# Performance work log

Hardware: AMD Instinct MI355X
Metric: run time of the kernel (lower is better)

Reference implementation:

```python
import jax, jax.numpy as jnp
import numpy as np

N = 50000      # nodes
DEG = 12       # in-degree per node
E = N * DEG    # 600000 edges
IN_FEATS = 256
H_FEATS = 128
NUM_LAYERS = 2
BN_EPS = 1e-5
PD_EPS = 1e-6  # torch pairwise_distance eps


def _batch_norm(x):
    # BatchNorm1d(affine=False) in training mode: per-feature batch stats, biased var
    m = x.mean(axis=0)
    v = ((x - m) ** 2).mean(axis=0)
    return (x - m) / jnp.sqrt(v + BN_EPS)


def setup_inputs() -> dict:
    key = jax.random.key(0)
    ks = jax.random.split(key, 6)
    x = jax.random.normal(ks[0], (N, IN_FEATS), dtype=jnp.float32)
    # xavier-uniform-like scales
    s_init = float(np.sqrt(6.0 / (IN_FEATS + H_FEATS)))
    s_h = float(np.sqrt(6.0 / (2 * H_FEATS)))
    W_init = jax.random.uniform(ks[1], (IN_FEATS, H_FEATS), jnp.float32, -s_init, s_init)
    W0 = jax.random.uniform(ks[2], (H_FEATS, H_FEATS), jnp.float32, -s_h, s_h)
    W1 = jax.random.uniform(ks[3], (H_FEATS, H_FEATS), jnp.float32, -s_h, s_h)
    b0 = jnp.zeros((H_FEATS,), jnp.float32)
    b1 = jnp.zeros((H_FEATS,), jnp.float32)
    src = jax.random.randint(ks[4], (E,), 0, N, dtype=jnp.int32)
    dst = jnp.repeat(jnp.arange(N, dtype=jnp.int32), DEG)  # every node has in-degree DEG
    return {"x": x, "W_init": W_init, "W0": W0, "b0": b0, "W1": W1, "b1": b1,
            "src": src, "dst": dst}


def _embed_nodes(x, W_init, Ws, bs, src, dst):
    # h = act(norm(x @ init_weight)); then GraphConv(norm='none') layers
    h = jax.nn.relu(_batch_norm(x @ W_init))
    for W, b in zip(Ws, bs):
        msg = h[src] @ W                       # [E, H]
        agg = jax.ops.segment_sum(msg, dst, num_segments=N)  # sum aggregation
        h = jax.nn.relu(_batch_norm(agg + b))
    return h


def _nonparametric_embedding(x, src, dst, deg):
    # GIN(apply_func=None, eps=-1, aggregator='mean') == mean of in-neighbors
    h = jax.nn.relu(_batch_norm(x))
    for _ in range(NUM_LAYERS):
        agg = jax.ops.segment_sum(h[src], dst, num_segments=N) / deg[:, None]
        h = jax.nn.relu(_batch_norm(agg))
    return h


def _mean_edge_dist(h, src, dst, deg):
    # apply_edges: pairwise_distance(src, dst); pull: scatter-mean onto dst
    d = jnp.linalg.norm(h[src] - h[dst] + PD_EPS, axis=1)  # [E]
    return jax.ops.segment_sum(d, dst, num_segments=N) / deg  # [N]


def reference(x, W_init, W0, b0, W1, b1, src, dst):
    deg = jnp.maximum(
        jax.ops.segment_sum(jnp.ones((E,), jnp.float32), dst, num_segments=N), 1.0)
    h_final = _embed_nodes(x, W_init, (W0, W1), (b0, b1), src, dst)
    # nonparametric target distances (detached in original)
    h_nonpar = _nonparametric_embedding(jax.lax.stop_gradient(x), src, dst, deg)
    d_nonpar = jax.lax.stop_gradient(_mean_edge_dist(h_nonpar, src, dst, deg))
    d_par = _mean_edge_dist(h_final, src, dst, deg)
    loss = jnp.mean((jnp.log(d_par) - jnp.log(d_nonpar)) ** 2)
    return (h_final, loss)
```

## Files before the change

### kernel.cpp

```cpp
#include <hip/hip_runtime.h>
#include <hip/hip_fp16.h>
#include <math.h>

#define DEG 12
#define BN_EPS 1e-5f
#define PD_EPS 1e-6f

using uint = unsigned int;

typedef _Float16 fp16x8 __attribute__((ext_vector_type(8)));
typedef float f32x2 __attribute__((ext_vector_type(2)));
typedef float f32x4 __attribute__((ext_vector_type(4)));

__device__ inline float2 h2f2(uint u) {
  __half2 h; __builtin_memcpy(&h, &u, 4);
  return __half22float2(h);
}
__device__ inline uint f2h2(float a, float b) {
  __half2 h = __floats2half2_rn(a, b);
  uint u; __builtin_memcpy(&u, &h, 4);
  return u;
}
__device__ inline f32x2 q2f_lo(uint u) { return __builtin_amdgcn_cvt_pk_f32_fp8(u, false); }
__device__ inline f32x2 q2f_hi(uint u) { return __builtin_amdgcn_cvt_pk_f32_fp8(u, true); }
__device__ inline uint f4_to_q(float a, float b, float c, float d) {
  uint w = 0;
  w = __builtin_amdgcn_cvt_pk_fp8_f32(a, b, w, false);
  w = __builtin_amdgcn_cvt_pk_fp8_f32(c, d, w, true);
  return w;
}

#define STATS_NB 256

template<int F>
__global__ __launch_bounds__(512) void stats_q_part(const uint* __restrict__ in,
                                                    float* __restrict__ parts, int M) {
  const int G = F / 8;
  __shared__ float redA[512 * 8];
  __shared__ float redB[512 * 8];
  int tid = threadIdx.x;
  int total = M * G;
  float s[8] = {0,0,0,0,0,0,0,0}, q[8] = {0,0,0,0,0,0,0,0};
  for (int i = blockIdx.x * 512 + tid; i < total; i += gridDim.x * 512) {
    uint2 raw = ((const uint2*)in)[i];
    f32x2 a = q2f_lo(raw.x), b = q2f_hi(raw.x), c = q2f_lo(raw.y), d = q2f_hi(raw.y);
    float v[8] = {a.x, a.y, b.x, b.y, c.x, c.y, d.x, d.y};
#pragma unroll
    for (int j = 0; j < 8; ++j) { s[j] += v[j]; q[j] += v[j] * v[j]; }
  }
#pragma unroll
  for (int j = 0; j < 8; ++j) { redA[tid * 8 + j] = s[j]; redB[tid * 8 + j] = q[j]; }
  __syncthreads();
  if (tid < F) {
    int c = tid >> 3, j = tid & 7;
    float as = 0.f, aq = 0.f;
#pragma unroll 4
    for (int r = 0; r < 512 / G; ++r) {
      as += redA[(r * G + c) * 8 + j];
      aq += redB[(r * G + c) * 8 + j];
    }
    parts[blockIdx.x * 2 * F + tid]     = as;
    parts[blockIdx.x * 2 * F + F + tid] = aq;
  }
}

template<int F>
__global__ __launch_bounds__(512) void stats_f_part(const float* __restrict__ in,
                                                    float* __restrict__ parts, int M) {
  const int G = F / 4;
  __shared__ float redA[512 * 4];
  __shared__ float redB[512 * 4];
  int tid = threadIdx.x;
  int total = M * G;
  float s[4] = {0,0,0,0}, q[4] = {0,0,0,0};
  for (int i = blockIdx.x * 512 + tid; i < total; i += gridDim.x * 512) {
    float4 v = ((const float4*)in)[i];
    float w[4] = {v.x, v.y, v.z, v.w};
#pragma unroll
    for (int j = 0; j < 4; ++j) { s[j] += w[j]; q[j] += w[j] * w[j]; }
  }
#pragma unroll
  for (int j = 0; j < 4; ++j) { redA[tid * 4 + j] = s[j]; redB[tid * 4 + j] = q[j]; }
  __syncthreads();
  if (tid < F) {
    int c = tid >> 2, j = tid & 3;
    float as = 0.f, aq = 0.f;
#pragma unroll 4
    for (int r = 0; r < 512 / G; ++r) {
      as += redA[(r * G + c) * 4 + j];
      aq += redB[(r * G + c) * 4 + j];
    }
    parts[blockIdx.x * 2 * F + tid]     = as;
    parts[blockIdx.x * 2 * F + F + tid] = aq;
  }
}

template<int F>
__global__ __launch_bounds__(1024) void stats_final(const float* __restrict__ parts,
                                                    int nb, int M, float* __restrict__ stats) {
  const int OUT = 2 * F;
  const int T   = 1024 / OUT;
  __shared__ float red[1024];
  int tid = threadIdx.x;
  int o = tid & (OUT - 1);
  int c = tid / OUT;
  float s = 0.f;
#pragma unroll 16
  for (int b = c; b < nb; b += T) s += parts[(size_t)b * OUT + o];
  red[tid] = s;
  __syncthreads();
  if (tid < OUT) {
    float acc = red[tid];
#pragma unroll
    for (int cc = 1; cc < T; ++cc) acc += red[cc * OUT + tid];
    red[tid] = acc;
  }
  __syncthreads();
  if (tid < F) {
    float mean = red[tid] / (float)M;
    float var  = red[F + tid] / (float)M - mean * mean;
    stats[tid]     = mean;
    stats[F + tid] = 1.0f / sqrtf(var + BN_EPS);
  }
}

__global__ void transpose_all(const float* __restrict__ Wi, const float* __restrict__ W0,
                              const float* __restrict__ W1, __half* __restrict__ WiT,
                              __half* __restrict__ W0T, __half* __restrict__ W1T) {
  int idx = blockIdx.x * 256 + threadIdx.x;
  if (idx < 32768) {
    int n = idx / 256, k = idx - n * 256;
    WiT[idx] = __float2half(Wi[(size_t)k * 128 + n]);
  } else if (idx < 49152) {
    int i = idx - 32768; int n = i / 128, k = i - n * 128;
    W0T[i] = __float2half(W0[(size_t)k * 128 + n]);
  } else if (idx < 65536) {
    int i = idx - 49152; int n = i / 128, k = i - n * 128;
    W1T[i] = __float2half(W1[(size_t)k * 128 + n]);
  }
}

__device__ __forceinline__ void colstats_epilogue_128(
    void* scratch, const f32x4* acc, int row0w, int M,
    float* __restrict__ parts, int bid, int tid, int kg, int r) {
  float* red = (float*)scratch;
  int slot = (tid >> 6) * 4 + kg;
  __syncthreads();
#pragma unroll
  for (int n = 0; n < 8; ++n) {
    float s = 0.f;
#pragma unroll
    for (int rr = 0; rr < 4; ++rr)
      if (row0w + kg * 4 + rr < M) s += acc[n][rr];
    red[slot * 128 + n * 16 + r] = s;
  }
  __syncthreads();
  if (tid < 128) {
    float s = 0.f;
#pragma unroll
    for (int i = 0; i < 16; ++i) s += red[i * 128 + tid];
    parts[(size_t)bid * 256 + tid] = s;
  }
  __syncthreads();
#pragma unroll
  for (int n = 0; n < 8; ++n) {
    float q = 0.f;
#pragma unroll
    for (int rr = 0; rr < 4; ++rr) {
      float v = (row0w + kg * 4 + rr < M) ? acc[n][rr] : 0.f;
      q += v * v;
    }
    red[slot * 128 + n * 16 + r] = q;
  }
  __syncthreads();
  if (tid < 128) {
    float q = 0.f;
#pragma unroll
    for (int i = 0; i < 16; ++i) q += red[i * 128 + tid];
    parts[(size_t)bid * 256 + 128 + tid] = q;
  }
}

__global__ __launch_bounds__(256) void gemm_x(
    const float* __restrict__ A, const float* __restrict__ stats,
    const __half* __restrict__ WT, __half* __restrict__ C,
    uint* __restrict__ xq, float* __restrict__ parts, int M) {
  __shared__ uint4 Bs4[64 * 32];
  char* Bs = (char*)Bs4;
  int tid = threadIdx.x;
  int wave = tid >> 6, lane = tid & 63;
  int row0 = blockIdx.x * 64 + wave * 16;
  int r = lane & 15, kg = lane >> 4;
  int arow = row0 + r; if (arow >= M) arow = M - 1;
  bool vrow = (row0 + r) < M;
  const float* Ap = A + (size_t)arow * 256 + kg * 8;

  fp16x8 af[8];
#pragma unroll
  for (int a = 0; a < 8; ++a) {
    int c0 = kg * 8 + a * 32;
    float4 lo = *(const float4*)(Ap + a * 32);
    float4 hi = *(const float4*)(Ap + a * 32 + 4);
    af[a][0] = (_Float16)lo.x; af[a][1] = (_Float16)lo.y;
    af[a][2] = (_Float16)lo.z; af[a][3] = (_Float16)lo.w;
    af[a][4] = (_Float16)hi.x; af[a][5] = (_Float16)hi.y;
    af[a][6] = (_Float16)hi.z; af[a][7] = (_Float16)hi.w;
    float4 m0 = *(const float4*)(stats + c0);
    float4 m1 = *(const float4*)(stats + c0 + 4);
    float4 v0 = *(const float4*)(stats + 256 + c0);
    float4 v1 = *(const float4*)(stats + 256 + c0 + 4);
    float w0 = fmaxf((lo.x - m0.x) * v0.x, 0.f);
    float w1 = fmaxf((lo.y - m0.y) * v0.y, 0.f);
    float w2 = fmaxf((lo.z - m0.z) * v0.z, 0.f);
    float w3 = fmaxf((lo.w - m0.w) * v0.w, 0.f);
    float w4 = fmaxf((hi.x - m1.x) * v1.x, 0.f);
    float w5 = fmaxf((hi.y - m1.y) * v1.y, 0.f);
    float w6 = fmaxf((hi.z - m1.z) * v1.z, 0.f);
    float w7 = fmaxf((hi.w - m1.w) * v1.w, 0.f);
    if (vrow) {
      uint2 q; q.x = f4_to_q(w0, w1, w2, w3); q.y = f4_to_q(w4, w5, w6, w7);
      ((uint2*)xq)[(size_t)arow * 32 + (c0 >> 3)] = q;
    }
  }

  f32x4 acc[8];
#pragma unroll
  for (int n = 0; n < 8; ++n) acc[n] = (f32x4){0.f, 0.f, 0.f, 0.f};
  const uint4* Wg = (const uint4*)WT;

#pragma unroll
  for (int ph = 0; ph < 2; ++ph) {
    __syncthreads();
#pragma unroll
    for (int i = 0; i < 8; ++i) {
      int idx = tid + i * 256;
      int rw = idx >> 5, c16 = idx & 31;
      *(uint4*)(Bs + rw * 512 + ((c16 * 16) ^ ((rw & 7) << 4))) = Wg[ph * 2048 + idx];
    }
    __syncthreads();
#pragma unroll
    for (int a = 0; a < 8; ++a) {
#pragma unroll
      for (int n4 = 0; n4 < 4; ++n4) {
        int rw = n4 * 16 + r;
        fp16x8 bf = *(const fp16x8*)(Bs + rw * 512 + ((kg * 16 + a * 64) ^ ((r & 7) << 4)));
        acc[ph * 4 + n4] = __builtin_amdgcn_mfma_f32_16x16x32_f16(af[a], bf, acc[ph * 4 + n4], 0, 0, 0);
      }
    }
  }
#pragma unroll
  for (int n = 0; n < 8; ++n) {
    int col = n * 16 + r;
#pragma unroll
    for (int rr = 0; rr < 4; ++rr) {
      int row = row0 + kg * 4 + rr;
      if (row < M) C[(size_t)row * 128 + col] = __float2half(acc[n][rr]);
    }
  }
  colstats_epilogue_128(Bs, acc, row0, M, parts, blockIdx.x, tid, kg, r);
}

__global__ __launch_bounds__(256) void gemm_128(
    const __half* __restrict__ A, const __half* __restrict__ WT,
    const float* __restrict__ bias, __half* __restrict__ C,
    float* __restrict__ parts, int M) {
  __shared__ uint4 Bs4[128 * 16];
  char* Bs = (char*)Bs4;
  int tid = threadIdx.x;
  const uint4* Wg = (const uint4*)WT;
#pragma unroll
  for (int i = 0; i < 8; ++i) {
    int idx = tid + i * 256;
    int rw = idx >> 4, c16 = idx & 15;
    *(uint4*)(Bs + rw * 256 + ((c16 * 16) ^ ((rw & 7) << 4))) = Wg[idx];
  }
  int wave = tid >> 6, lane = tid & 63;
  int row0 = blockIdx.x * 64 + wave * 16;
  int r = lane & 15, kg = lane >> 4;
  int arow = row0 + r; if (arow >= M) arow = M - 1;
  const _Float16* Ap = (const _Float16*)A + (size_t)arow * 128 + kg * 8;

  fp16x8 af[4];
#pragma unroll
  for (int a = 0; a < 4; ++a) af[a] = *(const fp16x8*)(Ap + a * 32);

  __syncthreads();
  f32x4 acc[8];
#pragma unroll
  for (int n = 0; n < 8; ++n) acc[n] = (f32x4){0.f, 0.f, 0.f, 0.f};
#pragma unroll
  for (int a = 0; a < 4; ++a) {
#pragma unroll
    for (int n = 0; n < 8; ++n) {
      int rw = n * 16 + r;
      fp16x8 bf = *(const fp16x8*)(Bs + rw * 256 + ((kg * 16 + a * 64) ^ ((r & 7) << 4)));
      acc[n] = __builtin_amdgcn_mfma_f32_16x16x32_f16(af[a], bf, acc[n], 0, 0, 0);
    }
  }
#pragma unroll
  for (int n = 0; n < 8; ++n) {
    int col = n * 16 + r;
    float bv = bias[col];
#pragma unroll
    for (int rr = 0; rr < 4; ++rr) {
      acc[n][rr] += bv;
      int row = row0 + kg * 4 + rr;
      if (row < M) C[(size_t)row * 128 + col] = __float2half(acc[n][rr]);
    }
  }
  colstats_epilogue_128(Bs, acc, row0, M, parts, blockIdx.x, tid, kg, r);
}

template<int F, bool BNRELU>
__global__ __launch_bounds__(256) void agg_n(
    const __half* __restrict__ H, const float* __restrict__ stats,
    const int* __restrict__ src, __half* __restrict__ outh,
    float scale, int n_nodes) {
  const int LPN = F / 8;
  const int NPB = 256 / LPN;
  int tid  = threadIdx.x;
  int g    = tid / LPN;
  int lig  = tid % LPN;
  int node = blockIdx.x * NPB + g;
  if (node >= n_nodes) return;
  float m[8], iv[8];
  if (BNRELU) {
#pragma unroll
    for (int j = 0; j < 8; ++j) {
      m[j]  = stats[lig * 8 + j];
      iv[j] = stats[F + lig * 8 + j];
    }
  }
  int lane = tid & 63;
  int grpStart = lane & (63 ^ (LPN - 1));
  int se = 0;
  if ((lane & (LPN - 1)) < DEG) se = src[node * DEG + (lane & (LPN - 1))];

  const uint4* HH = (const uint4*)H;
  float a[8] = {0,0,0,0,0,0,0,0};
#pragma unroll
  for (int e = 0; e < DEG; ++e) {
    int s = __shfl(se, grpStart + e);
    uint4 raw = HH[(size_t)s * LPN + lig];
    float2 v0 = h2f2(raw.x), v1 = h2f2(raw.y), v2 = h2f2(raw.z), v3 = h2f2(raw.w);
    float w[8] = {v0.x, v0.y, v1.x, v1.y, v2.x, v2.y, v3.x, v3.y};
    if (BNRELU) {
#pragma unroll
      for (int j = 0; j < 8; ++j) w[j] = fmaxf((w[j] - m[j]) * iv[j], 0.f);
    }
#pragma unroll
    for (int j = 0; j < 8; ++j) a[j] += w[j];
  }
  uint4 w;
  w.x = f2h2(a[0] * scale, a[1] * scale);
  w.y = f2h2(a[2] * scale, a[3] * scale);
  w.z = f2h2(a[4] * scale, a[5] * scale);
  w.w = f2h2(a[6] * scale, a[7] * scale);
  ((uint4*)outh)[(size_t)node * LPN + lig] = w;
}

template<int F, bool BNRELU>
__global__ __launch_bounds__(256) void agg_q(
    const uint* __restrict__ H, const float* __restrict__ stats,
    const int* __restrict__ src, uint* __restrict__ outq,
    float scale, int n_nodes) {
  const int LPN = F / 8;
  const int NPB = 256 / LPN;
  int tid  = threadIdx.x;
  int g    = tid / LPN;
  int lig  = tid % LPN;
  int node = blockIdx.x * NPB + g;
  if (node >= n_nodes) return;
  float m[8], iv[8];
  if (BNRELU) {
#pragma unroll
    for (int j = 0; j < 8; ++j) {
      m[j]  = stats[lig * 8 + j];
      iv[j] = stats[F + lig * 8 + j];
    }
  }
  int lane = tid & 63;
  int grpStart = lane & (63 ^ (LPN - 1));
  int se = 0;
  if ((lane & (LPN - 1)) < DEG) se = src[node * DEG + (lane & (LPN - 1))];

  const uint2* HH = (const uint2*)H;
  float a[8] = {0,0,0,0,0,0,0,0};
#pragma unroll
  for (int e = 0; e < DEG; ++e) {
    int s = __shfl(se, grpStart + e);
    uint2 raw = HH[(size_t)s * LPN + lig];
    f32x2 p0 = q2f_lo(raw.x), p1 = q2f_hi(raw.x), p2 = q2f_lo(raw.y), p3 = q2f_hi(raw.y);
    float w[8] = {p0.x, p0.y, p1.x, p1.y, p2.x, p2.y, p3.x, p3.y};
    if (BNRELU) {
#pragma unroll
      for (int j = 0; j < 8; ++j) w[j] = fmaxf((w[j] - m[j]) * iv[j], 0.f);
    }
#pragma unroll
    for (int j = 0; j < 8; ++j) a[j] += w[j];
  }
  uint2 w;
  w.x = f4_to_q(a[0] * scale, a[1] * scale, a[2] * scale, a[3] * scale);
  w.y = f4_to_q(a[4] * scale, a[5] * scale, a[6] * scale, a[7] * scale);
  ((uint2*)outq)[(size_t)node * LPN + lig] = w;
}

template<int F>
__global__ __launch_bounds__(256) void dist_q(
    const uint* __restrict__ H, const int* __restrict__ src,
    float* __restrict__ out, int n_nodes) {
  const int LPN = 16;
  const int NPB = 256 / LPN;
  const int NU2 = F / 128;
  int tid  = threadIdx.x;
  int g    = tid / LPN;
  int lig  = tid % LPN;
  int node = blockIdx.x * NPB + g;
  if (node >= n_nodes) return;
  int lane = tid & 63;
  int grpStart = lane & 48;
  int se = 0;
  if ((lane & 15) < DEG) se = src[node * DEG + (lane & 15)];

  const uint2* HH = (const uint2*)H;
  float oe[NU2 * 8];
#pragma unroll
  for (int k = 0; k < NU2; ++k) {
    uint2 o = HH[(size_t)node * (F / 8) + lig * NU2 + k];
    f32x2 p0 = q2f_lo(o.x), p1 = q2f_hi(o.x), p2 = q2f_lo(o.y), p3 = q2f_hi(o.y);
    oe[k*8+0] = PD_EPS - p0.x; oe[k*8+1] = PD_EPS - p0.y;
    oe[k*8+2] = PD_EPS - p1.x; oe[k*8+3] = PD_EPS - p1.y;
    oe[k*8+4] = PD_EPS - p2.x; oe[k*8+5] = PD_EPS - p2.y;
    oe[k*8+6] = PD_EPS - p3.x; oe[k*8+7] = PD_EPS - p3.y;
  }

  float dsum = 0.f;
#pragma unroll
  for (int e = 0; e < DEG; ++e) {
    int s = __shfl(se, grpStart + e);
    float sq = 0.f;
#pragma unroll
    for (int k = 0; k < NU2; ++k) {
      uint2 raw = HH[(size_t)s * (F / 8) + lig * NU2 + k];
      f32x2 p0 = q2f_lo(raw.x), p1 = q2f_hi(raw.x), p2 = q2f_lo(raw.y), p3 = q2f_hi(raw.y);
      float w[8] = {p0.x, p0.y, p1.x, p1.y, p2.x, p2.y, p3.x, p3.y};
#pragma unroll
      for (int j = 0; j < 8; ++j) {
        float d = w[j] + oe[k*8+j];
        sq = fmaf(d, d, sq);
      }
    }
#pragma unroll
    for (int mask = 1; mask < LPN; mask <<= 1) sq += __shfl_xor(sq, mask);
    dsum += sqrtf(sq);
  }
  if (lig == 0) out[node] = dsum * (1.0f / (float)DEG);
}

template<int F>
__global__ void bnrelu_q2q(const uint* __restrict__ in, const float* __restrict__ stats,
                           uint* __restrict__ out, int total1) {
  for (int idx = blockIdx.x * blockDim.x + threadIdx.x; idx < total1;
       idx += gridDim.x * blockDim.x) {
    uint raw = in[idx];
    int f0 = (idx & (F / 4 - 1)) * 4;
    f32x2 p0 = q2f_lo(raw), p1 = q2f_hi(raw);
    float w0 = fmaxf((p0.x - stats[f0+0]) * stats[F+f0+0], 0.f);
    float w1 = fmaxf((p0.y - stats[f0+1]) * stats[F+f0+1], 0.f);
    float w2 = fmaxf((p1.x - stats[f0+2]) * stats[F+f0+2], 0.f);
    float w3 = fmaxf((p1.y - stats[f0+3]) * stats[F+f0+3], 0.f);
    out[idx] = f4_to_q(w0, w1, w2, w3);
  }
}

template<int F>
__global__ void bnrelu_dual_h(const __half* __restrict__ in, const float* __restrict__ stats,
                              float* __restrict__ outf, uint* __restrict__ outq, int total8) {
  for (int idx = blockIdx.x * blockDim.x + threadIdx.x; idx < total8;
       idx += gridDim.x * blockDim.x) {
    uint4 raw = ((const uint4*)in)[idx];
    int f0 = (idx & (F / 8 - 1)) * 8;
    float2 v0 = h2f2(raw.x), v1 = h2f2(raw.y), v2 = h2f2(raw.z), v3 = h2f2(raw.w);
    float w0 = fmaxf((v0.x - stats[f0+0]) * stats[F+f0+0], 0.f);
    float w1 = fmaxf((v0.y - stats[f0+1]) * stats[F+f0+1], 0.f);
    float w2 = fmaxf((v1.x - stats[f0+2]) * stats[F+f0+2], 0.f);
    float w3 = fmaxf((v1.y - stats[f0+3]) * stats[F+f0+3], 0.f);
    float w4 = fmaxf((v2.x - stats[f0+4]) * stats[F+f0+4], 0.f);
    float w5 = fmaxf((v2.y - stats[f0+5]) * stats[F+f0+5], 0.f);
    float w6 = fmaxf((v3.x - stats[f0+6]) * stats[F+f0+6], 0.f);
    float w7 = fmaxf((v3.y - stats[f0+7]) * stats[F+f0+7], 0.f);
    ((float4*)outf)[idx * 2]     = make_float4(w0, w1, w2, w3);
    ((float4*)outf)[idx * 2 + 1] = make_float4(w4, w5, w6, w7);
    uint2 q; q.x = f4_to_q(w0, w1, w2, w3); q.y = f4_to_q(w4, w5, w6, w7);
    ((uint2*)outq)[idx] = q;
  }
}

__global__ void loss_partial(const float* __restrict__ dpar, const float* __restrict__ dnp,
                             float* __restrict__ parts, int n) {
  __shared__ float red[256];
  float acc = 0.f;
  for (int i = blockIdx.x * 256 + threadIdx.x; i < n; i += gridDim.x * 256) {
    float t = logf(dpar[i]) - logf(dnp[i]);
    acc += t * t;
  }
  red[threadIdx.x] = acc;
  __syncthreads();
  for (int s = 128; s; s >>= 1) {
    if (threadIdx.x < s) red[threadIdx.x] += red[threadIdx.x + s];
    __syncthreads();
  }
  if (threadIdx.x == 0) parts[blockIdx.x] = red[0];
}

__global__ void loss_final(const float* __restrict__ parts, int nb,
                           float* __restrict__ out, float inv_n) {
  if (threadIdx.x == 0) {
    float s = 0.f;
    for (int i = 0; i < nb; ++i) s += parts[i];
    *out = s * inv_n;
  }
}

extern "C" void kernel_launch(void* const* d_in, const int* in_sizes, int n_in,
                              void* d_out, int out_size, void* d_ws, size_t ws_size,
                              hipStream_t stream) {
  const float* x  = (const float*)d_in[0];
  const float* Wi = (const float*)d_in[1];
  const float* W0 = (const float*)d_in[2];
  const float* b0 = (const float*)d_in[3];
  const float* W1 = (const float*)d_in[4];
  const float* b1 = (const float*)d_in[5];
  const int*  src = (const int*)d_in[6];

  const int N = in_sizes[0] / 256;
  float* out = (float*)d_out;

  const int g64 = (N + 63) / 64;

  const size_t NF = (size_t)N * 128;
  float* S1 = (float*)d_ws;
  float* S2 = S1 + NF;
  float* S3 = S2 + NF;
  float* aux = S3 + NF;
  float* dpar   = aux;
  float* dnp    = dpar + N;
  float* parts  = dnp + N;
  float* s_x    = parts + 204800;
  float* s_y0   = s_x + 512;
  float* s_z1   = s_y0 + 256;
  float* s_z2   = s_z1 + 256;
  float* s_a1   = s_z2 + 256;
  float* s_a2   = s_a1 + 512;
  float* lparts = s_a2 + 512;
  __half* WiT   = (__half*)(lparts + 64);
  __half* W0T   = (__half*)(lparts + 64 + 16384);
  __half* W1T   = (__half*)(lparts + 64 + 24576);
  uint*   xq    = (uint*)(lparts + 64 + 32768);

  __half* y0h = (__half*)S1;
  __half* H0h = (__half*)S2;
  __half* z1h = (__half*)S1;
  __half* H1h = (__half*)S2;
  __half* z2h = (__half*)S3;
  uint* hq   = (uint*)S1;
  uint* A1q  = (uint*)S3;
  uint* A2q  = (uint*)S2;
  uint* A2nq = (uint*)S1;

  const int g128a = N / 16;
  const int gaggq = N / 8;
  const int gdist = N / 16;

  transpose_all<<<256, 256, 0, stream>>>(Wi, W0, W1, WiT, W0T, W1T);

  stats_f_part<256><<<STATS_NB, 512, 0, stream>>>(x, parts, N);
  stats_final<256><<<1, 1024, 0, stream>>>(parts, STATS_NB, N, s_x);

  gemm_x<<<g64, 256, 0, stream>>>(x, s_x, WiT, y0h, xq, parts, N);
  stats_final<128><<<1, 1024, 0, stream>>>(parts, g64, N, s_y0);
  agg_n<128, true><<<g128a, 256, 0, stream>>>(y0h, s_y0, src, H0h, 1.0f, N);
  gemm_128<<<g64, 256, 0, stream>>>(H0h, W0T, b0, z1h, parts, N);
  stats_final<128><<<1, 1024, 0, stream>>>(parts, g64, N, s_z1);
  agg_n<128, true><<<g128a, 256, 0, stream>>>(z1h, s_z1, src, H1h, 1.0f, N);
  gemm_128<<<g64, 256, 0, stream>>>(H1h, W1T, b1, z2h, parts, N);
  stats_final<128><<<1, 1024, 0, stream>>>(parts, g64, N, s_z2);
  bnrelu_dual_h<128><<<2048, 256, 0, stream>>>(z2h, s_z2, out, hq, N * 16);
  dist_q<128><<<gdist, 256, 0, stream>>>(hq, src, dpar, N);

  agg_q<256, false><<<gaggq, 256, 0, stream>>>(xq, nullptr, src, A1q, 1.0f / DEG, N);
  stats_q_part<256><<<STATS_NB, 512, 0, stream>>>(A1q, parts, N);
  stats_final<256><<<1, 1024, 0, stream>>>(parts, STATS_NB, N, s_a1);
  agg_q<256, true><<<gaggq, 256, 0, stream>>>(A1q, s_a1, src, A2q, 1.0f / DEG, N);
  stats_q_part<256><<<STATS_NB, 512, 0, stream>>>(A2q, parts, N);
  stats_final<256><<<1, 1024, 0, stream>>>(parts, STATS_NB, N, s_a2);
  bnrelu_q2q<256><<<2048, 256, 0, stream>>>(A2q, s_a2, A2nq, N * 64);
  dist_q<256><<<gdist, 256, 0, stream>>>(A2nq, src, dnp, N);

  loss_partial<<<64, 256, 0, stream>>>(dpar, dnp, lparts, N);
  loss_final<<<1, 64, 0, stream>>>(lparts, 64, out + (size_t)N * 128, 1.0f / (float)N);
}
```

Baseline: 275.2 us.

## Fuse BN-ReLU and loss partials into 256-wide distance kernel, widen agg loads

Drops the standalone BN+ReLU pass over the 256-feature nonparametric embedding by applying normalization inside the distance kernel for both the node and its neighbors. The same kernel also computes the log-squared loss partials, removing the separate dnp buffer and the loss_partial kernel, and loss_final becomes a parallel 1024-thread reduction. The 256-feature aggregation now uses 16 lanes per node with 16-byte loads instead of 32 lanes with 8-byte loads. This trades extra per-edge BN arithmetic for one fewer full read and write pass and fewer launches.

Result: slower. 293.2 us (+6.6%).

```diff
diff --git a/kernel.cpp b/kernel.cpp
--- a/kernel.cpp
+++ b/kernel.cpp
@@ -28,6 +28,12 @@
   w = __builtin_amdgcn_cvt_pk_fp8_f32(a, b, w, false);
   w = __builtin_amdgcn_cvt_pk_fp8_f32(c, d, w, true);
   return w;
+}
+__device__ inline void deq16(uint4 raw, float* w) {
+  f32x2 p0 = q2f_lo(raw.x), p1 = q2f_hi(raw.x), p2 = q2f_lo(raw.y), p3 = q2f_hi(raw.y);
+  f32x2 p4 = q2f_lo(raw.z), p5 = q2f_hi(raw.z), p6 = q2f_lo(raw.w), p7 = q2f_hi(raw.w);
+  w[0]=p0.x; w[1]=p0.y; w[2]=p1.x; w[3]=p1.y; w[4]=p2.x; w[5]=p2.y; w[6]=p3.x; w[7]=p3.y;
+  w[8]=p4.x; w[9]=p4.y; w[10]=p5.x; w[11]=p5.y; w[12]=p6.x; w[13]=p6.y; w[14]=p7.x; w[15]=p7.y;
 }
 
 #define STATS_NB 256
@@ -359,63 +365,61 @@
   ((uint4*)outh)[(size_t)node * LPN + lig] = w;
 }
 
-template<int F, bool BNRELU>
-__global__ __launch_bounds__(256) void agg_q(
-    const uint* __restrict__ H, const float* __restrict__ stats,
-    const int* __restrict__ src, uint* __restrict__ outq,
+template<bool BNRELU>
+__global__ __launch_bounds__(256) void agg_q4(
+    const uint4* __restrict__ H, const float* __restrict__ stats,
+    const int* __restrict__ src, uint4* __restrict__ outq,
     float scale, int n_nodes) {
-  const int LPN = F / 8;
-  const int NPB = 256 / LPN;
+  const int LPN = 16;
   int tid  = threadIdx.x;
-  int g    = tid / LPN;
-  int lig  = tid % LPN;
-  int node = blockIdx.x * NPB + g;
+  int g    = tid >> 4;
+  int lig  = tid & 15;
+  int node = blockIdx.x * 16 + g;
   if (node >= n_nodes) return;
-  float m[8], iv[8];
+  float m[16], iv[16];
   if (BNRELU) {
 #pragma unroll
-    for (int j = 0; j < 8; ++j) {
-      m[j]  = stats[lig * 8 + j];
-      iv[j] = stats[F + lig * 8 + j];
+    for (int j = 0; j < 16; ++j) {
+      m[j]  = stats[lig * 16 + j];
+      iv[j] = stats[256 + lig * 16 + j];
     }
   }
   int lane = tid & 63;
-  int grpStart = lane & (63 ^ (LPN - 1));
+  int grpStart = lane & 48;
   int se = 0;
-  if ((lane & (LPN - 1)) < DEG) se = src[node * DEG + (lane & (LPN - 1))];
-
-  const uint2* HH = (const uint2*)H;
-  float a[8] = {0,0,0,0,0,0,0,0};
+  if ((lane & 15) < DEG) se = src[node * DEG + (lane & 15)];
+
+  float a[16];
+#pragma unroll
+  for (int j = 0; j < 16; ++j) a[j] = 0.f;
 #pragma unroll
   for (int e = 0; e < DEG; ++e) {
     int s = __shfl(se, grpStart + e);
-    uint2 raw = HH[(size_t)s * LPN + lig];
-    f32x2 p0 = q2f_lo(raw.x), p1 = q2f_hi(raw.x), p2 = q2f_lo(raw.y), p3 = q2f_hi(raw.y);
-    float w[8] = {p0.x, p0.y, p1.x, p1.y, p2.x, p2.y, p3.x, p3.y};
+    uint4 raw = H[(size_t)s * LPN + lig];
+    float w[16]; deq16(raw, w);
     if (BNRELU) {
 #pragma unroll
-      for (int j = 0; j < 8; ++j) w[j] = fmaxf((w[j] - m[j]) * iv[j], 0.f);
-    }
-#pragma unroll
-    for (int j = 0; j < 8; ++j) a[j] += w[j];
-  }
-  uint2 w;
+      for (int j = 0; j < 16; ++j) w[j] = fmaxf((w[j] - m[j]) * iv[j], 0.f);
+    }
+#pragma unroll
+    for (int j = 0; j < 16; ++j) a[j] += w[j];
+  }
+  uint4 w;
   w.x = f4_to_q(a[0] * scale, a[1] * scale, a[2] * scale, a[3] * scale);
   w.y = f4_to_q(a[4] * scale, a[5] * scale, a[6] * scale, a[7] * scale);
-  ((uint2*)outq)[(size_t)node * LPN + lig] = w;
-}
-
-template<int F>
-__global__ __launch_bounds__(256) void dist_q(
+  w.z = f4_to_q(a[8] * scale, a[9] * scale, a[10] * scale, a[11] * scale);
+  w.w = f4_to_q(a[12] * scale, a[13] * scale, a[14] * scale, a[15] * scale);
+  outq[(size_t)node * LPN + lig] = w;
+}
+
+__global__ __launch_bounds__(256) void dist_q128(
     const uint* __restrict__ H, const int* __restrict__ src,
     float* __restrict__ out, int n_nodes) {
   const int LPN = 16;
-  const int NPB = 256 / LPN;
-  const int NU2 = F / 128;
   int tid  = threadIdx.x;
-  int g    = tid / LPN;
-  int lig  = tid % LPN;
-  int node = blockIdx.x * NPB + g;
+  int g    = tid >> 4;
+  int lig  = tid & 15;
+  int node = blockIdx.x * 16 + g;
   if (node >= n_nodes) return;
   int lane = tid & 63;
   int grpStart = lane & 48;
@@ -423,32 +427,23 @@
   if ((lane & 15) < DEG) se = src[node * DEG + (lane & 15)];
 
   const uint2* HH = (const uint2*)H;
-  float oe[NU2 * 8];
-#pragma unroll
-  for (int k = 0; k < NU2; ++k) {
-    uint2 o = HH[(size_t)node * (F / 8) + lig * NU2 + k];
-    f32x2 p0 = q2f_lo(o.x), p1 = q2f_hi(o.x), p2 = q2f_lo(o.y), p3 = q2f_hi(o.y);
-    oe[k*8+0] = PD_EPS - p0.x; oe[k*8+1] = PD_EPS - p0.y;
-    oe[k*8+2] = PD_EPS - p1.x; oe[k*8+3] = PD_EPS - p1.y;
-    oe[k*8+4] = PD_EPS - p2.x; oe[k*8+5] = PD_EPS - p2.y;
-    oe[k*8+6] = PD_EPS - p3.x; oe[k*8+7] = PD_EPS - p3.y;
-  }
+  uint2 o = HH[(size_t)node * 16 + lig];
+  f32x2 p0 = q2f_lo(o.x), p1 = q2f_hi(o.x), p2 = q2f_lo(o.y), p3 = q2f_hi(o.y);
+  float oe[8] = {PD_EPS - p0.x, PD_EPS - p0.y, PD_EPS - p1.x, PD_EPS - p1.y,
+                 PD_EPS - p2.x, PD_EPS - p2.y, PD_EPS - p3.x, PD_EPS - p3.y};
 
   float dsum = 0.f;
 #pragma unroll
   for (int e = 0; e < DEG; ++e) {
     int s = __shfl(se, grpStart + e);
+    uint2 raw = HH[(size_t)s * 16 + lig];
+    f32x2 q0 = q2f_lo(raw.x), q1 = q2f_hi(raw.x), q2 = q2f_lo(raw.y), q3 = q2f_hi(raw.y);
+    float w[8] = {q0.x, q0.y, q1.x, q1.y, q2.x, q2.y, q3.x, q3.y};
     float sq = 0.f;
 #pragma unroll
-    for (int k = 0; k < NU2; ++k) {
-      uint2 raw = HH[(size_t)s * (F / 8) + lig * NU2 + k];
-      f32x2 p0 = q2f_lo(raw.x), p1 = q2f_hi(raw.x), p2 = q2f_lo(raw.y), p3 = q2f_hi(raw.y);
-      float w[8] = {p0.x, p0.y, p1.x, p1.y, p2.x, p2.y, p3.x, p3.y};
-#pragma unroll
-      for (int j = 0; j < 8; ++j) {
-        float d = w[j] + oe[k*8+j];
-        sq = fmaf(d, d, sq);
-      }
+    for (int j = 0; j < 8; ++j) {
+      float d = w[j] + oe[j];
+      sq = fmaf(d, d, sq);
     }
 #pragma unroll
     for (int mask = 1; mask < LPN; mask <<= 1) sq += __shfl_xor(sq, mask);
@@ -457,19 +452,61 @@
   if (lig == 0) out[node] = dsum * (1.0f / (float)DEG);
 }
 
-template<int F>
-__global__ void bnrelu_q2q(const uint* __restrict__ in, const float* __restrict__ stats,
-                           uint* __restrict__ out, int total1) {
-  for (int idx = blockIdx.x * blockDim.x + threadIdx.x; idx < total1;
-       idx += gridDim.x * blockDim.x) {
-    uint raw = in[idx];
-    int f0 = (idx & (F / 4 - 1)) * 4;
-    f32x2 p0 = q2f_lo(raw), p1 = q2f_hi(raw);
-    float w0 = fmaxf((p0.x - stats[f0+0]) * stats[F+f0+0], 0.f);
-    float w1 = fmaxf((p0.y - stats[f0+1]) * stats[F+f0+1], 0.f);
-    float w2 = fmaxf((p1.x - stats[f0+2]) * stats[F+f0+2], 0.f);
-    float w3 = fmaxf((p1.y - stats[f0+3]) * stats[F+f0+3], 0.f);
-    out[idx] = f4_to_q(w0, w1, w2, w3);
+__global__ __launch_bounds__(256) void dist256_loss(
+    const uint4* __restrict__ H, const float* __restrict__ stats,
+    const int* __restrict__ src, const float* __restrict__ dpar,
+    float* __restrict__ lparts, int n_nodes) {
+  __shared__ float red[16];
+  const int LPN = 16;
+  int tid  = threadIdx.x;
+  int g    = tid >> 4;
+  int lig  = tid & 15;
+  int node = blockIdx.x * 16 + g;
+  int lane = tid & 63;
+  int grpStart = lane & 48;
+  int se = 0;
+  if ((lane & 15) < DEG) se = src[node * DEG + (lane & 15)];
+
+  float m[16], iv[16];
+#pragma unroll
+  for (int j = 0; j < 16; ++j) {
+    m[j]  = stats[lig * 16 + j];
+    iv[j] = stats[256 + lig * 16 + j];
+  }
+  uint4 o = H[(size_t)node * LPN + lig];
+  float ow[16]; deq16(o, ow);
+  float oe[16];
+#pragma unroll
+  for (int j = 0; j < 16; ++j)
+    oe[j] = PD_EPS - fmaxf((ow[j] - m[j]) * iv[j], 0.f);
+
+  float dsum = 0.f;
+#pragma unroll
+  for (int e = 0; e < DEG; ++e) {
+    int s = __shfl(se, grpStart + e);
+    uint4 raw = H[(size_t)s * LPN + lig];
+    float w[16]; deq16(raw, w);
+    float sq = 0.f;
+#pragma unroll
+    for (int j = 0; j < 16; ++j) {
+      float d = fmaxf((w[j] - m[j]) * iv[j], 0.f) + oe[j];
+      sq = fmaf(d, d, sq);
+    }
+#pragma unroll
+    for (int mask = 1; mask < LPN; mask <<= 1) sq += __shfl_xor(sq, mask);
+    dsum += sqrtf(sq);
+  }
+  if (lig == 0) {
+    float d = dsum * (1.0f / (float)DEG);
+    float t = logf(dpar[node]) - logf(d);
+    red[g] = t * t;
+  }
+  __syncthreads();
+  if (tid == 0) {
+    float s = 0.f;
+#pragma unroll
+    for (int i = 0; i < 16; ++i) s += red[i];
+    lparts[blockIdx.x] = s;
   }
 }
 
@@ -496,30 +533,19 @@
   }
 }
 
-__global__ void loss_partial(const float* __restrict__ dpar, const float* __restrict__ dnp,
-                             float* __restrict__ parts, int n) {
-  __shared__ float red[256];
-  float acc = 0.f;
-  for (int i = blockIdx.x * 256 + threadIdx.x; i < n; i += gridDim.x * 256) {
-    float t = logf(dpar[i]) - logf(dnp[i]);
-    acc += t * t;
-  }
-  red[threadIdx.x] = acc;
-  __syncthreads();
-  for (int s = 128; s; s >>= 1) {
-    if (threadIdx.x < s) red[threadIdx.x] += red[threadIdx.x + s];
+__global__ __launch_bounds__(1024) void loss_final(const float* __restrict__ parts, int nb,
+                                                   float* __restrict__ out, float inv_n) {
+  __shared__ float red[1024];
+  int tid = threadIdx.x;
+  float s = 0.f;
+  for (int i = tid; i < nb; i += 1024) s += parts[i];
+  red[tid] = s;
+  __syncthreads();
+  for (int st = 512; st; st >>= 1) {
+    if (tid < st) red[tid] += red[tid + st];
     __syncthreads();
   }
-  if (threadIdx.x == 0) parts[blockIdx.x] = red[0];
-}
-
-__global__ void loss_final(const float* __restrict__ parts, int nb,
-                           float* __restrict__ out, float inv_n) {
-  if (threadIdx.x == 0) {
-    float s = 0.f;
-    for (int i = 0; i < nb; ++i) s += parts[i];
-    *out = s * inv_n;
-  }
+  if (tid == 0) *out = red[0] * inv_n;
 }
 
 extern "C" void kernel_launch(void* const* d_in, const int* in_sizes, int n_in,
@@ -544,8 +570,7 @@
   float* S3 = S2 + NF;
   float* aux = S3 + NF;
   float* dpar   = aux;
-  float* dnp    = dpar + N;
-  float* parts  = dnp + N;
+  float* parts  = dpar + N;
   float* s_x    = parts + 204800;
   float* s_y0   = s_x + 512;
   float* s_z1   = s_y0 + 256;
@@ -553,24 +578,22 @@
   float* s_a1   = s_z2 + 256;
   float* s_a2   = s_a1 + 512;
   float* lparts = s_a2 + 512;
-  __half* WiT   = (__half*)(lparts + 64);
-  __half* W0T   = (__half*)(lparts + 64 + 16384);
-  __half* W1T   = (__half*)(lparts + 64 + 24576);
-  uint*   xq    = (uint*)(lparts + 64 + 32768);
+  __half* WiT   = (__half*)(lparts + 3200);
+  __half* W0T   = (__half*)(lparts + 3200 + 16384);
+  __half* W1T   = (__half*)(lparts + 3200 + 24576);
+  uint*   xq    = (uint*)(lparts + 3200 + 32768);
 
   __half* y0h = (__half*)S1;
   __half* H0h = (__half*)S2;
   __half* z1h = (__half*)S1;
   __half* H1h = (__half*)S2;
   __half* z2h = (__half*)S3;
-  uint* hq   = (uint*)S1;
-  uint* A1q  = (uint*)S3;
-  uint* A2q  = (uint*)S2;
-  uint* A2nq = (uint*)S1;
+  uint* hq  = (uint*)S1;
+  uint* A1q = (uint*)S3;
+  uint* A2q = (uint*)S2;
 
   const int g128a = N / 16;
-  const int gaggq = N / 8;
-  const int gdist = N / 16;
+  const int gq16  = N / 16;
 
   transpose_all<<<256, 256, 0, stream>>>(Wi, W0, W1, WiT, W0T, W1T);
 
@@ -586,17 +609,15 @@
   gemm_128<<<g64, 256, 0, stream>>>(H1h, W1T, b1, z2h, parts, N);
   stats_final<128><<<1, 1024, 0, stream>>>(parts, g64, N, s_z2);
   bnrelu_dual_h<128><<<2048, 256, 0, stream>>>(z2h, s_z2, out, hq, N * 16);
-  dist_q<128><<<gdist, 256, 0, stream>>>(hq, src, dpar, N);
-
-  agg_q<256, false><<<gaggq, 256, 0, stream>>>(xq, nullptr, src, A1q, 1.0f / DEG, N);
+  dist_q128<<<gq16, 256, 0, stream>>>(hq, src, dpar, N);
+
+  agg_q4<false><<<gq16, 256, 0, stream>>>((const uint4*)xq, nullptr, src, (uint4*)A1q, 1.0f / DEG, N);
   stats_q_part<256><<<STATS_NB, 512, 0, stream>>>(A1q, parts, N);
   stats_final<256><<<1, 1024, 0, stream>>>(parts, STATS_NB, N, s_a1);
-  agg_q<256, true><<<gaggq, 256, 0, stream>>>(A1q, s_a1, src, A2q, 1.0f / DEG, N);
+  agg_q4<true><<<gq16, 256, 0, stream>>>((const uint4*)A1q, s_a1, src, (uint4*)A2q, 1.0f / DEG, N);
   stats_q_part<256><<<STATS_NB, 512, 0, stream>>>(A2q, parts, N);
   stats_final<256><<<1, 1024, 0, stream>>>(parts, STATS_NB, N, s_a2);
-  bnrelu_q2q<256><<<2048, 256, 0, stream>>>(A2q, s_a2, A2nq, N * 64);
-  dist_q<256><<<gdist, 256, 0, stream>>>(A2nq, src, dnp, N);
-
-  loss_partial<<<64, 256, 0, stream>>>(dpar, dnp, lparts, N);
-  loss_final<<<1, 64, 0, stream>>>(lparts, 64, out + (size_t)N * 128, 1.0f / (float)N);
-}
+  dist256_loss<<<gq16, 256, 0, stream>>>((const uint4*)A2q, s_a2, src, dpar, lparts, N);
+
+  loss_final<<<1, 1024, 0, stream>>>(lparts, gq16, out + (size_t)N * 128, 1.0f / (float)N);
+}
```
